# Optimization experiments

Measured on AMD Instinct MI355X. Metric: run time of the kernel, lower is better.

The kernel has to match this reference:

```python
import jax, jax.numpy as jnp
import numpy as np

NUM_HEADS = 8
GS = 7  # group_size (window) side

def _relative_position_index():
    # static index table, matches the torch meshgrid('ij') construction
    coords = np.stack(np.meshgrid(np.arange(GS), np.arange(GS), indexing='ij'))  # (2,GS,GS)
    cf = coords.reshape(2, -1)                                 # (2, 49)
    rel = cf[:, :, None] - cf[:, None, :]                      # (2, 49, 49)
    rel = rel.transpose(1, 2, 0).copy()                        # (49, 49, 2)
    rel[..., 0] += GS - 1
    rel[..., 1] += GS - 1
    rel[..., 0] *= 2 * GS - 1
    return rel.sum(-1)                                         # (49, 49) in [0, 169)

REL_INDEX = jnp.asarray(_relative_position_index())

def setup_inputs() -> dict:
    key = jax.random.key(0)
    ks = jax.random.split(key, 5)
    B, N, C = 2048, 49, 256
    HID = 64
    return {
        'q': jax.random.normal(ks[0], (B, N, C), dtype=jnp.float32),
        'k': jax.random.normal(ks[1], (B, N, C), dtype=jnp.float32),
        'v': jax.random.normal(ks[2], (B, N, C), dtype=jnp.float32),
        'W1': jax.random.normal(ks[3], (2, HID), dtype=jnp.float32) * 0.1,
        'b1': jnp.zeros((HID,), dtype=jnp.float32),
        'W2': jax.random.normal(ks[4], (HID, NUM_HEADS), dtype=jnp.float32) * 0.1,
        'b2': jnp.zeros((NUM_HEADS,), dtype=jnp.float32),
        'H': 56,
        'W': 56,
    }

def _bias_table(W1, b1, W2, b2):
    # biases: (2*GS-1)^2 relative offsets, dpb_pos modeled as 2-layer MLP 2->HID->heads
    r = jnp.arange(1 - GS, GS, dtype=jnp.float32)
    bh, bw = jnp.meshgrid(r, r, indexing='ij')
    biases = jnp.stack([bh.ravel(), bw.ravel()], axis=1)       # (169, 2)
    pos = jax.nn.relu(biases @ W1 + b1) @ W2 + b2              # (169, heads)
    return pos[REL_INDEX].transpose(2, 0, 1)                   # (heads, 49, 49)

def reference(q, k, v, W1, b1, W2, b2, H, W):
    B, N, C = q.shape
    h = NUM_HEADS
    d = C // h
    scale = d ** -0.5
    qh = q.reshape(B, N, h, d)
    kh = k.reshape(B, N, h, d)
    vh = v.reshape(B, N, h, d)
    attn = jnp.einsum('bihd,bjhd->bhij', qh, kh) * scale       # (B,h,N,N)
    bias = _bias_table(W1, b1, W2, b2)                         # (h,49,49)
    if H == 7 and W == 7:
        attn = attn.at[:, :, 0:GS * GS, 0:GS * GS].add(bias[None])
    else:
        attn = attn + bias[None]
    attn = jax.nn.softmax(attn, axis=-1)
    out = jnp.einsum('bhij,bjhd->bihd', attn, vh).reshape(B, N, C)
    return out
```

## Files before the change

### kernel.cpp

```cpp
#include <hip/hip_runtime.h>
#include <hip/hip_bf16.h>

typedef __attribute__((ext_vector_type(8))) _Float16 f16x8;
typedef __attribute__((ext_vector_type(4))) float f32x4;

#define NWIN 49
#define NH 8
#define CCH 256
#define PROW 72

__device__ __forceinline__ uint cvt2_u32(float a, float b) {
    auto t = __builtin_amdgcn_cvt_pkrtz(a, b);
    return *(uint*)&t;
}
__device__ __forceinline__ f16x8 mk8(uint a, uint b, uint c, uint d) {
    union { uint u[4]; f16x8 v; } x;
    x.u[0] = a; x.u[1] = b; x.u[2] = c; x.u[3] = d;
    return x.v;
}
__device__ __forceinline__ ushort4 pack4(uint a, uint b) {
    union { uint u[2]; ushort4 s; } x;
    x.u[0] = a; x.u[1] = b;
    return x.s;
}

__global__ void pos_mlp_kernel(const float* __restrict__ W1, const float* __restrict__ b1,
                               const float* __restrict__ W2, const float* __restrict__ b2,
                               float* __restrict__ pos) {
    int idx = blockIdx.x * blockDim.x + threadIdx.x;
    if (idx >= 169) return;
    float bh = (float)(idx / 13) - 6.0f;
    float bw = (float)(idx % 13) - 6.0f;
    float outv[NH];
#pragma unroll
    for (int t = 0; t < NH; ++t) outv[t] = b2[t];
    for (int u = 0; u < 64; ++u) {
        float hv = fmaf(bh, W1[u], fmaf(bw, W1[64 + u], b1[u]));
        hv = fmaxf(hv, 0.0f);
#pragma unroll
        for (int t = 0; t < NH; ++t) outv[t] = fmaf(hv, W2[u * NH + t], outv[t]);
    }
#pragma unroll
    for (int t = 0; t < NH; ++t) pos[idx * NH + t] = outv[t];
}

__global__ void bias_frag_kernel(const float* __restrict__ pos, float* __restrict__ bfrag) {
    int blk = blockIdx.x;
    int it = blk & 3, jt = (blk >> 2) & 3, h = blk >> 4;
    int lane = threadIdx.x;
    int g = lane >> 4, l15 = lane & 15;
    int i = it * 16 + l15;
    float4 v;
    float* vp = (float*)&v;
#pragma unroll
    for (int r = 0; r < 4; ++r) {
        int j = jt * 16 + g * 4 + r;
        float val;
        if (j >= NWIN) val = -1e30f;
        else if (i >= NWIN) val = 0.0f;
        else {
            int rel = (i / 7 - j / 7 + 6) * 13 + (i % 7 - j % 7 + 6);
            val = pos[rel * NH + h] * 1.4426950408889634f;
        }
        vp[r] = val;
    }
    *(float4*)(bfrag + (size_t)blk * 256 + lane * 4) = v;
}

__global__ __launch_bounds__(512, 2) void attn_kernel(
    const float* __restrict__ q, const float* __restrict__ k,
    const float* __restrict__ v, const float* __restrict__ bfrag,
    float* __restrict__ out) {
    __shared__ __align__(16) ushort sP[8][64 * PROW];

    const int nper = (int)(gridDim.x >> 3);
    const int b = ((int)blockIdx.x & 7) * nper + ((int)blockIdx.x >> 3);

    const int tid = threadIdx.x;
    const int w = tid >> 6, lane = tid & 63;
    const int h = w;
    const int g = lane >> 4, l15 = lane & 15;
    const size_t base = (size_t)b * (NWIN * CCH) + h * 32;
    ushort* myP = sP[w];

    float4 kraw[4][2], qraw[4][2];
#pragma unroll
    for (int t = 0; t < 4; ++t) {
        int row = t * 16 + l15;
        int rc = row < NWIN ? row : NWIN - 1;
        const float* kp = k + base + (size_t)rc * CCH + g * 8;
        const float* qp = q + base + (size_t)rc * CCH + g * 8;
        kraw[t][0] = *(const float4*)kp; kraw[t][1] = *(const float4*)(kp + 4);
        qraw[t][0] = *(const float4*)qp; qraw[t][1] = *(const float4*)(qp + 4);
    }
    float vv[2][2][8];
#pragma unroll
    for (int ks = 0; ks < 2; ++ks)
#pragma unroll
        for (int nt = 0; nt < 2; ++nt)
#pragma unroll
            for (int e = 0; e < 8; ++e) {
                int j = ks * 32 + g * 8 + e;
                int jc = j < NWIN ? j : NWIN - 1;
                vv[ks][nt][e] = v[base + (size_t)jc * CCH + nt * 16 + l15];
            }
    f32x4 bb[4][4];
#pragma unroll
    for (int jt = 0; jt < 4; ++jt)
#pragma unroll
        for (int it = 0; it < 4; ++it)
            bb[jt][it] = *(const f32x4*)(bfrag + (size_t)((h * 4 + jt) * 4 + it) * 256 + lane * 4);

#pragma unroll
    for (int t = 0; t < 4; ++t)
        asm volatile("" :: "v"(kraw[t][0].x), "v"(kraw[t][1].x),
                           "v"(qraw[t][0].x), "v"(qraw[t][1].x));

    f16x8 ka16[4], qb16[4];
#pragma unroll
    for (int t = 0; t < 4; ++t) {
        float4 a = kraw[t][0], c = kraw[t][1];
        ka16[t] = mk8(cvt2_u32(a.x, a.y), cvt2_u32(a.z, a.w),
                      cvt2_u32(c.x, c.y), cvt2_u32(c.z, c.w));
        float4 d = qraw[t][0], e = qraw[t][1];
        qb16[t] = mk8(cvt2_u32(d.x, d.y), cvt2_u32(d.z, d.w),
                      cvt2_u32(e.x, e.y), cvt2_u32(e.z, e.w));
    }

    f32x4 acc[4][4];
#pragma unroll
    for (int jt = 0; jt < 4; ++jt)
#pragma unroll
        for (int it = 0; it < 4; ++it) {
            f32x4 a = {0.f, 0.f, 0.f, 0.f};
            acc[jt][it] = __builtin_amdgcn_mfma_f32_16x16x32_f16(ka16[jt], qb16[it], a, 0, 0, 0);
        }

#pragma unroll
    for (int jt = 0; jt < 4; ++jt)
        asm volatile("" :: "v"(bb[jt][0].x), "v"(bb[jt][1].x),
                           "v"(bb[jt][2].x), "v"(bb[jt][3].x));

    const float scale2 = 0.17677669529663687f * 1.4426950408889634f;
#pragma unroll
    for (int it = 0; it < 4; ++it) {
        float p[16];
        float s = 0.0f;
#pragma unroll
        for (int jt = 0; jt < 4; ++jt)
#pragma unroll
            for (int r = 0; r < 4; ++r) {
                float e = __builtin_amdgcn_exp2f(fmaf(acc[jt][it][r], scale2, bb[jt][it][r]));
                p[jt * 4 + r] = e;
                s += e;
            }
        s += __shfl_xor(s, 16);
        s += __shfl_xor(s, 32);
        const float inv = 1.0f / s;
#pragma unroll
        for (int jt = 0; jt < 4; ++jt) {
            uint a01 = cvt2_u32(p[jt * 4 + 0] * inv, p[jt * 4 + 1] * inv);
            uint a23 = cvt2_u32(p[jt * 4 + 2] * inv, p[jt * 4 + 3] * inv);
            *(ushort4*)&myP[(it * 16 + l15) * PROW + jt * 16 + g * 4] = pack4(a01, a23);
        }
    }

#pragma unroll
    for (int ks = 0; ks < 2; ++ks)
#pragma unroll
        for (int nt = 0; nt < 2; ++nt)
            asm volatile("" :: "v"(vv[ks][nt][0]), "v"(vv[ks][nt][1]),
                               "v"(vv[ks][nt][2]), "v"(vv[ks][nt][3]),
                               "v"(vv[ks][nt][4]), "v"(vv[ks][nt][5]),
                               "v"(vv[ks][nt][6]), "v"(vv[ks][nt][7]));
    f16x8 bv[2][2];
#pragma unroll
    for (int ks = 0; ks < 2; ++ks)
#pragma unroll
        for (int nt = 0; nt < 2; ++nt)
            bv[ks][nt] = mk8(cvt2_u32(vv[ks][nt][0], vv[ks][nt][1]),
                             cvt2_u32(vv[ks][nt][2], vv[ks][nt][3]),
                             cvt2_u32(vv[ks][nt][4], vv[ks][nt][5]),
                             cvt2_u32(vv[ks][nt][6], vv[ks][nt][7]));

    f32x4 oacc[4][2];
#pragma unroll
    for (int mt = 0; mt < 4; ++mt)
#pragma unroll
        for (int nt = 0; nt < 2; ++nt) oacc[mt][nt] = (f32x4){0.f, 0.f, 0.f, 0.f};
#pragma unroll
    for (int ks = 0; ks < 2; ++ks)
#pragma unroll
        for (int mt = 0; mt < 4; ++mt) {
            f16x8 pa = *(const f16x8*)&myP[(mt * 16 + l15) * PROW + ks * 32 + g * 8];
#pragma unroll
            for (int nt = 0; nt < 2; ++nt)
                oacc[mt][nt] = __builtin_amdgcn_mfma_f32_16x16x32_f16(pa, bv[ks][nt], oacc[mt][nt], 0, 0, 0);
        }

#pragma unroll
    for (int mt = 0; mt < 4; ++mt)
#pragma unroll
        for (int r = 0; r < 4; ++r) {
            int i = mt * 16 + g * 4 + r;
            if (i < NWIN) {
                float* op = out + base + (size_t)i * CCH + l15;
                op[0]  = oacc[mt][0][r];
                op[16] = oacc[mt][1][r];
            }
        }
}

extern "C" void kernel_launch(void* const* d_in, const int* in_sizes, int n_in,
                              void* d_out, int out_size, void* d_ws, size_t ws_size,
                              hipStream_t stream) {
    const float* q  = (const float*)d_in[0];
    const float* k  = (const float*)d_in[1];
    const float* v  = (const float*)d_in[2];
    const float* W1 = (const float*)d_in[3];
    const float* b1 = (const float*)d_in[4];
    const float* W2 = (const float*)d_in[5];
    const float* b2 = (const float*)d_in[6];

    float* pos   = (float*)d_ws;
    float* bfrag = (float*)((char*)d_ws + 8192);
    float* out   = (float*)d_out;

    const int B = in_sizes[0] / (NWIN * CCH);

    pos_mlp_kernel<<<1, 192, 0, stream>>>(W1, b1, W2, b2, pos);
    bias_frag_kernel<<<128, 64, 0, stream>>>(pos, bfrag);
    attn_kernel<<<B, 512, 0, stream>>>(q, k, v, bfrag, out);
}
```

Measured before the change: 111.0 us.

## Keep softmax probabilities in registers and use 16x16x16 MFMA for PV

Removes the shared-memory staging of the probability matrix. The softmax output fragments are reused directly as A operands of 16x16x16 f16 MFMAs, with V loaded in a matching 4-row-per-lane layout. This drops the LDS write/read round trip and frees LDS so occupancy can rise to 3 blocks per CU via launch bounds. The trade-off is twice as many smaller MFMA instructions and tighter register limits under the higher occupancy target. The bias loads are also moved to after the QK MFMAs.

```diff
diff --git a/kernel.cpp b/kernel.cpp
--- a/kernel.cpp
+++ b/kernel.cpp
@@ -1,27 +1,26 @@
 #include <hip/hip_runtime.h>
-#include <hip/hip_bf16.h>
-
+
+typedef __attribute__((ext_vector_type(4))) _Float16 f16x4;
 typedef __attribute__((ext_vector_type(8))) _Float16 f16x8;
 typedef __attribute__((ext_vector_type(4))) float f32x4;
 
 #define NWIN 49
 #define NH 8
 #define CCH 256
-#define PROW 72
 
 __device__ __forceinline__ uint cvt2_u32(float a, float b) {
     auto t = __builtin_amdgcn_cvt_pkrtz(a, b);
     return *(uint*)&t;
+}
+__device__ __forceinline__ f16x4 mk4(uint a, uint b) {
+    union { uint u[2]; f16x4 v; } x;
+    x.u[0] = a; x.u[1] = b;
+    return x.v;
 }
 __device__ __forceinline__ f16x8 mk8(uint a, uint b, uint c, uint d) {
     union { uint u[4]; f16x8 v; } x;
     x.u[0] = a; x.u[1] = b; x.u[2] = c; x.u[3] = d;
     return x.v;
-}
-__device__ __forceinline__ ushort4 pack4(uint a, uint b) {
-    union { uint u[2]; ushort4 s; } x;
-    x.u[0] = a; x.u[1] = b;
-    return x.s;
 }
 
 __global__ void pos_mlp_kernel(const float* __restrict__ W1, const float* __restrict__ b1,
@@ -67,12 +66,10 @@
     *(float4*)(bfrag + (size_t)blk * 256 + lane * 4) = v;
 }
 
-__global__ __launch_bounds__(512, 2) void attn_kernel(
+__global__ __launch_bounds__(512, 3) void attn_kernel(
     const float* __restrict__ q, const float* __restrict__ k,
     const float* __restrict__ v, const float* __restrict__ bfrag,
     float* __restrict__ out) {
-    __shared__ __align__(16) ushort sP[8][64 * PROW];
-
     const int nper = (int)(gridDim.x >> 3);
     const int b = ((int)blockIdx.x & 7) * nper + ((int)blockIdx.x >> 3);
 
@@ -81,7 +78,6 @@
     const int h = w;
     const int g = lane >> 4, l15 = lane & 15;
     const size_t base = (size_t)b * (NWIN * CCH) + h * 32;
-    ushort* myP = sP[w];
 
     float4 kraw[4][2], qraw[4][2];
 #pragma unroll
@@ -93,23 +89,17 @@
         kraw[t][0] = *(const float4*)kp; kraw[t][1] = *(const float4*)(kp + 4);
         qraw[t][0] = *(const float4*)qp; qraw[t][1] = *(const float4*)(qp + 4);
     }
-    float vv[2][2][8];
-#pragma unroll
-    for (int ks = 0; ks < 2; ++ks)
+    float vv[4][2][4];
+#pragma unroll
+    for (int jt = 0; jt < 4; ++jt)
 #pragma unroll
         for (int nt = 0; nt < 2; ++nt)
 #pragma unroll
-            for (int e = 0; e < 8; ++e) {
-                int j = ks * 32 + g * 8 + e;
+            for (int r = 0; r < 4; ++r) {
+                int j = jt * 16 + 4 * g + r;
                 int jc = j < NWIN ? j : NWIN - 1;
-                vv[ks][nt][e] = v[base + (size_t)jc * CCH + nt * 16 + l15];
+                vv[jt][nt][r] = v[base + (size_t)jc * CCH + nt * 16 + l15];
             }
-    f32x4 bb[4][4];
-#pragma unroll
-    for (int jt = 0; jt < 4; ++jt)
-#pragma unroll
-        for (int it = 0; it < 4; ++it)
-            bb[jt][it] = *(const f32x4*)(bfrag + (size_t)((h * 4 + jt) * 4 + it) * 256 + lane * 4);
 
 #pragma unroll
     for (int t = 0; t < 4; ++t)
@@ -136,12 +126,15 @@
             acc[jt][it] = __builtin_amdgcn_mfma_f32_16x16x32_f16(ka16[jt], qb16[it], a, 0, 0, 0);
         }
 
-#pragma unroll
-    for (int jt = 0; jt < 4; ++jt)
-        asm volatile("" :: "v"(bb[jt][0].x), "v"(bb[jt][1].x),
-                           "v"(bb[jt][2].x), "v"(bb[jt][3].x));
+    f32x4 bb[4][4];
+#pragma unroll
+    for (int jt = 0; jt < 4; ++jt)
+#pragma unroll
+        for (int it = 0; it < 4; ++it)
+            bb[jt][it] = *(const f32x4*)(bfrag + (size_t)((h * 4 + jt) * 4 + it) * 256 + lane * 4);
 
     const float scale2 = 0.17677669529663687f * 1.4426950408889634f;
+    f16x4 pfrag[4][4];
 #pragma unroll
     for (int it = 0; it < 4; ++it) {
         float p[16];
@@ -158,30 +151,22 @@
         s += __shfl_xor(s, 32);
         const float inv = 1.0f / s;
 #pragma unroll
-        for (int jt = 0; jt < 4; ++jt) {
-            uint a01 = cvt2_u32(p[jt * 4 + 0] * inv, p[jt * 4 + 1] * inv);
-            uint a23 = cvt2_u32(p[jt * 4 + 2] * inv, p[jt * 4 + 3] * inv);
-            *(ushort4*)&myP[(it * 16 + l15) * PROW + jt * 16 + g * 4] = pack4(a01, a23);
-        }
-    }
-
-#pragma unroll
-    for (int ks = 0; ks < 2; ++ks)
+        for (int jt = 0; jt < 4; ++jt)
+            pfrag[jt][it] = mk4(cvt2_u32(p[jt * 4 + 0] * inv, p[jt * 4 + 1] * inv),
+                                cvt2_u32(p[jt * 4 + 2] * inv, p[jt * 4 + 3] * inv));
+    }
+
+#pragma unroll
+    for (int jt = 0; jt < 4; ++jt)
+        asm volatile("" :: "v"(vv[jt][0][0]), "v"(vv[jt][0][3]),
+                           "v"(vv[jt][1][0]), "v"(vv[jt][1][3]));
+    f16x4 vfrag[4][2];
+#pragma unroll
+    for (int jt = 0; jt < 4; ++jt)
 #pragma unroll
         for (int nt = 0; nt < 2; ++nt)
-            asm volatile("" :: "v"(vv[ks][nt][0]), "v"(vv[ks][nt][1]),
-                               "v"(vv[ks][nt][2]), "v"(vv[ks][nt][3]),
-                               "v"(vv[ks][nt][4]), "v"(vv[ks][nt][5]),
-                               "v"(vv[ks][nt][6]), "v"(vv[ks][nt][7]));
-    f16x8 bv[2][2];
-#pragma unroll
-    for (int ks = 0; ks < 2; ++ks)
-#pragma unroll
-        for (int nt = 0; nt < 2; ++nt)
-            bv[ks][nt] = mk8(cvt2_u32(vv[ks][nt][0], vv[ks][nt][1]),
-                             cvt2_u32(vv[ks][nt][2], vv[ks][nt][3]),
-                             cvt2_u32(vv[ks][nt][4], vv[ks][nt][5]),
-                             cvt2_u32(vv[ks][nt][6], vv[ks][nt][7]));
+            vfrag[jt][nt] = mk4(cvt2_u32(vv[jt][nt][0], vv[jt][nt][1]),
+                                cvt2_u32(vv[jt][nt][2], vv[jt][nt][3]));
 
     f32x4 oacc[4][2];
 #pragma unroll
@@ -189,14 +174,13 @@
 #pragma unroll
         for (int nt = 0; nt < 2; ++nt) oacc[mt][nt] = (f32x4){0.f, 0.f, 0.f, 0.f};
 #pragma unroll
-    for (int ks = 0; ks < 2; ++ks)
-#pragma unroll
-        for (int mt = 0; mt < 4; ++mt) {
-            f16x8 pa = *(const f16x8*)&myP[(mt * 16 + l15) * PROW + ks * 32 + g * 8];
+    for (int jt = 0; jt < 4; ++jt)
+#pragma unroll
+        for (int mt = 0; mt < 4; ++mt)
 #pragma unroll
             for (int nt = 0; nt < 2; ++nt)
-                oacc[mt][nt] = __builtin_amdgcn_mfma_f32_16x16x32_f16(pa, bv[ks][nt], oacc[mt][nt], 0, 0, 0);
-        }
+                oacc[mt][nt] = __builtin_amdgcn_mfma_f32_16x16x16f16(pfrag[jt][mt], vfrag[jt][nt],
+                                                                     oacc[mt][nt], 0, 0, 0);
 
 #pragma unroll
     for (int mt = 0; mt < 4; ++mt)
```

Result: faster. 108.6 us (-2.1%).
